# Kernel tuning notes

Measured on AMD Instinct MI355X. Metric: run time of the kernel, lower is better.

## Reference

```python
import jax, jax.numpy as jnp
import numpy as np

E, K, CAP = 8, 2, 48
RD, NC = 64, 10
LOAD_PEN, MIN_USE, TEMP = 2.0, 0.05, 1.0


def _conv(x, w):
    return jax.lax.conv_general_dilated(x, w, (1, 1), 'SAME',
                                        dimension_numbers=('NCHW', 'OIHW', 'NCHW'))


def _bn(x, g, b):
    # eval-mode BatchNorm2d with running_mean=0, running_var=1, eps=1e-5
    s = g / np.float32(np.sqrt(1.0 + 1e-5))
    return x * s[:, None, None] + b[:, None, None]


def _maxpool2(x):
    return jax.lax.reduce_window(x, -jnp.inf, jax.lax.max,
                                 (1, 1, 2, 2), (1, 1, 2, 2), 'VALID')


def setup_inputs() -> dict:
    key = jax.random.key(0)
    ks = iter(jax.random.split(key, 40))
    n = lambda shape, s=0.1: jax.random.normal(next(ks), shape, jnp.float32) * s
    B = 256
    return dict(
        x=jax.random.normal(next(ks), (B, 3, 32, 32), jnp.float32),
        # routing trunk
        tw1=n((32, 3, 3, 3)), tg1=jnp.ones(32), tb1=jnp.zeros(32),
        tw2=n((32, 32, 3, 3)), tg2=jnp.ones(32), tb2=jnp.zeros(32),
        tfw=n((RD, 128)), tfb=jnp.zeros(RD),
        # gate MLP
        gw1=n((RD // 2, RD)), gb1=jnp.zeros(RD // 2),
        gw2=n((E, RD // 2)), gb2=jnp.zeros(E),
        # per-expert feature extractors (stacked over E)
        ew1=n((E, 32, 3, 3, 3)), eg1=jnp.ones((E, 32)), eb1=jnp.zeros((E, 32)),
        ew2=n((E, 64, 32, 3, 3)), eg2=jnp.ones((E, 64)), eb2=jnp.zeros((E, 64)),
        ew3=n((E, 128, 64, 3, 3)), eg3=jnp.ones((E, 128)), eb3=jnp.zeros((E, 128)),
        efw=n((E, 128, 128)), efb=jnp.zeros((E, 128)),
        # per-expert classifiers (stacked over E)
        cw1=n((E, 64, 128)), cb1=jnp.zeros((E, 64)),
        cw2=n((E, NC, 64)), cb2=jnp.zeros((E, NC)),
    )


def _forward(x, tw1, tg1, tb1, tw2, tg2, tb2, tfw, tfb, gw1, gb1, gw2, gb2,
             ew1, eg1, eb1, ew2, eg2, eb2, ew3, eg3, eb3, efw, efb,
             cw1, cb1, cw2, cb2):
    B = x.shape[0]
    # ---- routing trunk ----
    h = jax.nn.relu(_bn(_conv(x, tw1), tg1, tb1))
    h = jax.nn.relu(_bn(_conv(h, tw2), tg2, tb2))
    h = _maxpool2(h)                                   # [B,32,16,16]
    h = h.reshape(B, 32, 2, 8, 2, 8).mean((3, 5))      # AdaptiveAvgPool2d(2)
    rf = jax.nn.relu(h.reshape(B, 128) @ tfw.T + tfb)  # [B,RD]
    # ---- gate ----
    scores = (jax.nn.relu(rf @ gw1.T + gb1) @ gw2.T + gb2) / TEMP  # [B,E]
    usage = jnp.ones(E, jnp.float32) / E               # expert_usage_ema buffer
    boost = jnp.where(usage < MIN_USE, (MIN_USE - usage) * 10.0, 0.0)
    balanced = scores + boost[None] - LOAD_PEN * usage[None]
    # ---- capacity-constrained top-k routing (eval: sample_order = arange) ----
    _, tk = jax.lax.top_k(balanced, K)                 # [B,K] int32

    def step(loads, tki):
        lt = loads[tki]                                # [K] loads of this sample's top-k
        avail = lt < CAP
        idx = jnp.where(jnp.any(avail), jnp.argmax(avail), jnp.argmin(lt))
        chosen = tki[idx]
        return loads.at[chosen].add(1.0), chosen

    _, chosen = jax.lax.scan(step, jnp.zeros(E, jnp.float32), tk)
    D = jax.nn.one_hot(chosen, E, dtype=bool)          # [B,E] dispatch mask

    # ---- experts: run each expert on the full batch, zero out unassigned ----
    def expert(w1, g1, b1, w2, g2, b2, w3, g3, b3, fw, fb, c1w, c1b, c2w, c2b):
        h = _maxpool2(jax.nn.relu(_bn(_conv(x, w1), g1, b1)))   # [B,32,16,16]
        h = _maxpool2(jax.nn.relu(_bn(_conv(h, w2), g2, b2)))   # [B,64,8,8]
        h = jax.nn.relu(_bn(_conv(h, w3), g3, b3)).mean((2, 3)) # GAP -> [B,128]
        f = jax.nn.relu(h @ fw.T + fb)
        return jax.nn.relu(f @ c1w.T + c1b) @ c2w.T + c2b        # [B,NC]

    outs = jax.vmap(expert)(ew1, eg1, eb1, ew2, eg2, eb2, ew3, eg3, eb3,
                            efw, efb, cw1, cb1, cw2, cb2)        # [E,B,NC]
    expert_outputs = jnp.where(D.T[:, :, None], outs, 0.0).transpose(1, 0, 2)  # [B,E,NC]

    # ---- combine via softmax over dispatched scores ----
    masked = jnp.where(D, balanced, -jnp.inf)
    rw = jax.nn.softmax(masked, axis=1) * D
    rw = rw / (rw.sum(1, keepdims=True) + 1e-12)
    final = jnp.einsum('be,bec->bc', rw, expert_outputs)         # [B,NC]
    return final, balanced, D


def reference(x, tw1, tg1, tb1, tw2, tg2, tb2, tfw, tfb, gw1, gb1, gw2, gb2,
              ew1, eg1, eb1, ew2, eg2, eb2, ew3, eg3, eb3, efw, efb,
              cw1, cb1, cw2, cb2):
    return _forward(x, tw1, tg1, tb1, tw2, tg2, tb2, tfw, tfb,
                    gw1, gb1, gw2, gb2, ew1, eg1, eb1, ew2, eg2, eb2,
                    ew3, eg3, eb3, efw, efb, cw1, cb1, cw2, cb2)
```

## Files before the change

kernel.cpp:

```cpp
#include <hip/hip_runtime.h>
#include <hip/hip_bf16.h>
#include <math.h>


#define BN_RS (1.0f / sqrtf(1.00001f))

typedef __attribute__((ext_vector_type(8))) short short8;
typedef __attribute__((ext_vector_type(4))) float floatx4;

static __device__ __forceinline__ ushort f2bf(float f) {
  unsigned u = __float_as_uint(f);
  unsigned r = (u + 0x7fffu + ((u >> 16) & 1u)) >> 16;
  return (ushort)r;
}
static __device__ __forceinline__ float bf2f(ushort h) {
  return __uint_as_float((unsigned)h << 16);
}

#define WS_TFP    0
#define WS_TK     262144
#define WS_W2H    264192
#define WS_W2L    282624
#define WS_EW2B   301056
#define WS_EW3B   595968

__global__ __launch_bounds__(256) void prep_kernel(
    const float* __restrict__ tw2, const float* __restrict__ ew2,
    const float* __restrict__ ew3, ushort* __restrict__ w2h,
    ushort* __restrict__ w2l, ushort* __restrict__ ew2b,
    ushort* __restrict__ ew3b)
{
  const int j = blockIdx.x * 256 + threadIdx.x;
  if (j < 9216) {
    int tap = j >> 10, oc = (j >> 5) & 31, ic = j & 31;
    float v = tw2[oc*288 + ic*9 + tap];
    ushort h = f2bf(v);
    w2h[j] = h;
    w2l[j] = f2bf(v - bf2f(h));
  } else if (j < 27648) {
    const int jj = (j - 9216) * 8;
    int e = jj / 18432, r2 = jj % 18432;
    int tap = r2 / 2048, r3 = r2 % 2048;
    int oc = r3 / 32, ic0 = r3 % 32;
    const float* src = &ew2[e*18432 + oc*288 + ic0*9 + tap];
    short8 o;
    #pragma unroll
    for (int k = 0; k < 8; ++k) o[k] = (short)f2bf(src[k*9]);
    *(short8*)&ew2b[jj] = o;
  } else if (j < 101376) {
    const int jj = (j - 27648) * 8;
    int e = jj / 73728, r2 = jj % 73728;
    int tap = r2 / 8192, r3 = r2 % 8192;
    int oc = r3 / 64, ic0 = r3 % 64;
    const float* src = &ew3[e*73728 + oc*576 + ic0*9 + tap];
    short8 o;
    #pragma unroll
    for (int k = 0; k < 8; ++k) o[k] = (short)f2bf(src[k*9]);
    *(short8*)&ew3b[jj] = o;
  }
}

__global__ __launch_bounds__(256) void trunk_kernel(
    const float* __restrict__ x, const float* __restrict__ tw1,
    const float* __restrict__ tg1, const float* __restrict__ tb1,
    const ushort* __restrict__ w2h, const ushort* __restrict__ w2l,
    const float* __restrict__ tg2, const float* __restrict__ tb2,
    float* __restrict__ tfp)
{
  __shared__ __align__(16) ushort smu[17696];
  float* smf = (float*)&smu[14400];
  const int t = threadIdx.x, blk = blockIdx.x;
  const int b = blk >> 3, rs = (blk >> 1) & 3, ch = blk & 1;
  const int r0 = rs * 8, c0 = ch * 16;

  {
    uint4 z = {0, 0, 0, 0};
    for (int j = t; j < 1800; j += 256) ((uint4*)smu)[j] = z;
  }
  for (int j = t; j < 720; j += 256) {
    int ic = j / 240, rem = j % 240, rr = rem / 20, c = rem % 20;
    int gy = r0 - 2 + rr, gx = c0 - 2 + c;
    float v = 0.f;
    if (gy >= 0 && gy < 32 && gx >= 0 && gx < 32)
      v = x[b*3072 + ic*1024 + gy*32 + gx];
    smf[j] = v;
  }
  for (int j = t; j < 864; j += 256) {
    int oc = j / 27, r = j % 27, ic = r / 9, k = r % 9;
    smf[720 + ic*288 + k*32 + oc] = tw1[j];
  }
  if (t < 32) { smf[1584 + t] = tg1[t]*BN_RS; smf[1584 + 32 + t] = tb1[t]; }
  __syncthreads();

  for (int it = 0; it < 2; ++it) {
    const int item = it*256 + t;
    if (item < 320) {
      const int oc = item & 31, rr = item >> 5;
      const int grow = r0 - 1 + rr;
      if (grow >= 0 && grow < 32) {
        float acc[18];
        #pragma unroll
        for (int c = 0; c < 18; ++c) acc[c] = 0.f;
        #pragma unroll 1
        for (int ic = 0; ic < 3; ++ic) {
          #pragma unroll 1
          for (int ky = 0; ky < 3; ++ky) {
            float wk[3];
            #pragma unroll
            for (int kx = 0; kx < 3; ++kx)
              wk[kx] = smf[720 + ic*288 + (ky*3 + kx)*32 + oc];
            const float* srow = &smf[ic*240 + (rr + ky)*20];
            float v[20];
            #pragma unroll
            for (int j4 = 0; j4 < 5; ++j4) {
              float4 q = *(const float4*)&srow[4*j4];
              v[4*j4] = q.x; v[4*j4+1] = q.y; v[4*j4+2] = q.z; v[4*j4+3] = q.w;
            }
            #pragma unroll
            for (int kx = 0; kx < 3; ++kx)
              #pragma unroll
              for (int c = 0; c < 18; ++c)
                acc[c] = fmaf(wk[kx], v[c+kx], acc[c]);
          }
        }
        const float s = smf[1584 + oc], bo = smf[1584 + 32 + oc];
        #pragma unroll
        for (int c = 0; c < 18; ++c) {
          const int gcol = c0 - 1 + c;
          float va = 0.f;
          if (gcol >= 0 && gcol < 32)
            va = fmaxf(fmaf(acc[c], s, bo), 0.f);
          ushort h = f2bf(va);
          ushort lo = f2bf(va - bf2f(h));
          const int ui = (rr*18 + c)*40 + oc;
          smu[ui] = h;
          smu[7200 + ui] = lo;
        }
      }
    }
  }
  __syncthreads();

  const int w4 = t >> 6, l = t & 63, col = l & 15, quad = l >> 4;
  const int nt = w4 & 1, yh = w4 >> 1;
  floatx4 acc2[4];
  #pragma unroll
  for (int y = 0; y < 4; ++y)
    #pragma unroll
    for (int i = 0; i < 4; ++i) acc2[y][i] = 0.f;

  #pragma unroll
  for (int dx = 0; dx < 3; ++dx) {
    #pragma unroll
    for (int dy = 0; dy < 3; ++dy) {
      const int wi = (dy*3 + dx)*1024 + (nt*16 + col)*32 + quad*8;
      short8 bh = *(const short8*)&w2h[wi];
      short8 bl = *(const short8*)&w2l[wi];
      #pragma unroll
      for (int y = 0; y < 4; ++y) {
        const int idx = ((yh*4 + y + dy)*18 + col + dx)*40 + quad*8;
        short8 ah = *(const short8*)&smu[idx];
        short8 al = *(const short8*)&smu[7200 + idx];
        acc2[y] = __builtin_amdgcn_mfma_f32_16x16x32_bf16(ah, bh, acc2[y], 0, 0, 0);
        acc2[y] = __builtin_amdgcn_mfma_f32_16x16x32_bf16(ah, bl, acc2[y], 0, 0, 0);
        acc2[y] = __builtin_amdgcn_mfma_f32_16x16x32_bf16(al, bh, acc2[y], 0, 0, 0);
      }
    }
  }

  {
    const int oc = nt*16 + col;
    const float s2 = tg2[oc]*BN_RS, bo2 = tb2[oc];
    float psum = 0.f;
    #pragma unroll
    for (int yp = 0; yp < 2; ++yp)
      #pragma unroll
      for (int i2 = 0; i2 < 2; ++i2) {
        float v00 = fmaxf(fmaf(acc2[2*yp][2*i2],     s2, bo2), 0.f);
        float v01 = fmaxf(fmaf(acc2[2*yp][2*i2+1],   s2, bo2), 0.f);
        float v10 = fmaxf(fmaf(acc2[2*yp+1][2*i2],   s2, bo2), 0.f);
        float v11 = fmaxf(fmaf(acc2[2*yp+1][2*i2+1], s2, bo2), 0.f);
        psum += fmaxf(fmaxf(v00, v01), fmaxf(v10, v11));
      }
    psum += __shfl_xor(psum, 16);
    psum += __shfl_xor(psum, 32);
    if (yh == 1 && quad == 0) smf[nt*32 + col] = psum;
    __syncthreads();
    if (yh == 0 && quad == 0) {
      float tot = psum + smf[nt*32 + col];
      tfp[b*256 + (rs*2 + ch)*32 + oc] = tot;
    }
  }
}

__global__ __launch_bounds__(64) void gate_kernel(
    const float* __restrict__ tfp, const float* __restrict__ tfw, const float* __restrict__ tfb,
    const float* __restrict__ gw1, const float* __restrict__ gb1,
    const float* __restrict__ gw2, const float* __restrict__ gb2,
    float* __restrict__ outBal, int* __restrict__ tk)
{
  __shared__ float feat[128], rf[64], g1[32], bal[8];
  const int b = blockIdx.x, t = threadIdx.x;
  #pragma unroll
  for (int h = 0; h < 2; ++h) {
    const int f = t + 64*h;
    const int oc = f >> 2, qy = (f >> 1) & 1, qx = f & 1;
    feat[f] = (tfp[b*256 + (4*qy + qx)*32 + oc] +
               tfp[b*256 + (4*qy + 2 + qx)*32 + oc]) * (1.f/64.f);
  }
  __syncthreads();
  {
    float a = tfb[t];
    const float4* wp = (const float4*)&tfw[t*128];
    #pragma unroll 8
    for (int i4 = 0; i4 < 32; ++i4) {
      float4 wv = wp[i4];
      a = fmaf(wv.x, feat[4*i4], a);   a = fmaf(wv.y, feat[4*i4+1], a);
      a = fmaf(wv.z, feat[4*i4+2], a); a = fmaf(wv.w, feat[4*i4+3], a);
    }
    rf[t] = fmaxf(a, 0.f);
  }
  __syncthreads();
  if (t < 32) {
    float a = gb1[t];
    const float4* wp = (const float4*)&gw1[t*64];
    #pragma unroll
    for (int i4 = 0; i4 < 16; ++i4) {
      float4 wv = wp[i4];
      a = fmaf(wv.x, rf[4*i4], a);   a = fmaf(wv.y, rf[4*i4+1], a);
      a = fmaf(wv.z, rf[4*i4+2], a); a = fmaf(wv.w, rf[4*i4+3], a);
    }
    g1[t] = fmaxf(a, 0.f);
  }
  __syncthreads();
  if (t < 8) {
    float a = gb2[t];
    const float4* wp = (const float4*)&gw2[t*32];
    #pragma unroll
    for (int i4 = 0; i4 < 8; ++i4) {
      float4 wv = wp[i4];
      a = fmaf(wv.x, g1[4*i4], a);   a = fmaf(wv.y, g1[4*i4+1], a);
      a = fmaf(wv.z, g1[4*i4+2], a); a = fmaf(wv.w, g1[4*i4+3], a);
    }
    const float v = a - 0.25f;
    bal[t] = v;
    outBal[b*8 + t] = v;
  }
  __syncthreads();
  if (t == 0) {
    int t0 = 0; float b0 = bal[0];
    #pragma unroll
    for (int e2 = 1; e2 < 8; ++e2) if (bal[e2] > b0) { b0 = bal[e2]; t0 = e2; }
    int t1 = -1; float b1 = -3.4e38f;
    #pragma unroll
    for (int e2 = 0; e2 < 8; ++e2) if (e2 != t0 && bal[e2] > b1) { b1 = bal[e2]; t1 = e2; }
    tk[b*2] = t0; tk[b*2 + 1] = t1;
  }
}

#define XA_IMG  0
#define XA_FEAT 3600
#define XA_SFF  3728
#define XA_SGG  3856
#define XA_XF   9040
#define XA_W1F  12508
#define XA_BN1F 13372
#define XA_SC   9040
__global__ __launch_bounds__(512, 2) void expALL_kernel(
    const float* __restrict__ x, const int* __restrict__ tk,
    const float* __restrict__ ew1, const float* __restrict__ eg1,
    const float* __restrict__ eb1, const ushort* __restrict__ ew2b,
    const float* __restrict__ eg2, const float* __restrict__ eb2,
    const ushort* __restrict__ ew3b, const float* __restrict__ eg3,
    const float* __restrict__ eb3, const float* __restrict__ efw,
    const float* __restrict__ efb, const float* __restrict__ cw1,
    const float* __restrict__ cb1, const float* __restrict__ cw2,
    const float* __restrict__ cb2, float* __restrict__ outF,
    float* __restrict__ outD)
{
  __shared__ __align__(16) ushort smu[27296];
  __shared__ int stk[512];
  __shared__ int sch;
  float* smf = (float*)smu;
  const int t = threadIdx.x, b = blockIdx.x;
  const int w8 = t >> 6, l = t & 63;
  const int col = l & 15, quad = l >> 4;

  stk[t] = tk[t];
  __syncthreads();
  if (t == 0) {
    unsigned long long Lp = 0ull;
    int chv = 0;
    for (int i = 0; i <= b; ++i) {
      const int a = stk[2*i], c = stk[2*i+1];
      const int la = (int)((Lp >> (a*8)) & 0xFFull);
      const int lc = (int)((Lp >> (c*8)) & 0xFFull);
      chv = (la < 48) ? a : ((lc < 48) ? c : ((la <= lc) ? a : c));
      Lp += 1ull << (chv*8);
    }
    sch = chv;
  } else {
    uint4 z; z.x = 0; z.y = 0; z.z = 0; z.w = 0;
    for (int j = t-1; j < 1620; j += 511) ((uint4*)smu)[j] = z;
    for (int j = t-1; j < 3468; j += 511) {
      int ic = j / 1156, rem = j % 1156, p = rem / 34, cpd = rem % 34;
      int gy = p - 1, gx = cpd - 1;
      float v = 0.f;
      if (gy >= 0 && gy < 32 && gx >= 0 && gx < 32) v = x[b*3072 + ic*1024 + gy*32 + gx];
      smf[XA_XF + j] = v;
    }
  }
  __syncthreads();
  const int e = sch;
  if (t < 8) outD[b*8 + t] = (t == e) ? 1.f : 0.f;

  const int ntile = w8 & 3, mhalf = w8 >> 2;
  short8 w2f[9];
  {
    const int oc2 = ntile*16 + col;
    #pragma unroll
    for (int tap = 0; tap < 9; ++tap)
      w2f[tap] = *(const short8*)&ew2b[(e*9 + tap)*2048 + oc2*32 + quad*8];
  }

  for (int j = t; j < 864; j += 512) {
    int oc = j / 27, r = j % 27, ic = r / 9, k = r % 9;
    smf[XA_W1F + ic*288 + k*32 + oc] = ew1[e*864 + j];
  }
  if (t < 32) { smf[XA_BN1F + t] = eg1[e*32 + t]*BN_RS; smf[XA_BN1F + 32 + t] = eb1[e*32 + t]; }
  __syncthreads();

  {
    const int g = t >> 5, c = t & 31;
    for (int rs = 0; rs < 4; ++rs) {
      const int r0 = rs * 8;
      float acc[2][8];
      #pragma unroll
      for (int o = 0; o < 2; ++o)
        #pragma unroll
        for (int r = 0; r < 8; ++r) acc[o][r] = 0.f;
      for (int ic = 0; ic < 3; ++ic) {
        float w[2][9];
        #pragma unroll
        for (int k = 0; k < 9; ++k) {
          float2 wv = *(const float2*)&smf[XA_W1F + ic*288 + k*32 + 2*g];
          w[0][k] = wv.x; w[1][k] = wv.y;
        }
        const float* src = &smf[XA_XF + ic*1156 + r0*34 + c];
        #pragma unroll
        for (int rr = 0; rr < 10; ++rr) {
          const float i0 = src[rr*34], i1 = src[rr*34 + 1], i2 = src[rr*34 + 2];
          #pragma unroll
          for (int dr = 0; dr < 3; ++dr) {
            const int r = rr - dr;
            if (r < 0 || r > 7) continue;
            #pragma unroll
            for (int o = 0; o < 2; ++o) {
              acc[o][r] = fmaf(w[o][dr*3+0], i0, acc[o][r]);
              acc[o][r] = fmaf(w[o][dr*3+1], i1, acc[o][r]);
              acc[o][r] = fmaf(w[o][dr*3+2], i2, acc[o][r]);
            }
          }
        }
      }
      #pragma unroll
      for (int o = 0; o < 2; ++o) {
        const int oc = 2*g + o;
        const float s = smf[XA_BN1F + oc], bo = smf[XA_BN1F + 32 + oc];
        float m[4];
        #pragma unroll
        for (int pr = 0; pr < 4; ++pr) {
          float v0 = fmaxf(fmaf(acc[o][2*pr],   s, bo), 0.f);
          float v1 = fmaxf(fmaf(acc[o][2*pr+1], s, bo), 0.f);
          m[pr] = fmaxf(v0, v1);
        }
        #pragma unroll
        for (int pr = 0; pr < 4; ++pr) {
          float nb = __shfl_xor(m[pr], 1);
          m[pr] = fmaxf(m[pr], nb);
        }
        if (!(c & 1)) {
          const int pc = c >> 1;
          #pragma unroll
          for (int pr = 0; pr < 4; ++pr)
            smu[XA_IMG + ((rs*4 + pr + 1)*18 + (pc + 1))*40 + oc] = f2bf(m[pr]);
        }
      }
    }
  }
  __syncthreads();

  const int oc3 = w8*16 + col;
  short8 w3f[9][2];
  #pragma unroll
  for (int tap = 0; tap < 9; ++tap)
    #pragma unroll
    for (int ks = 0; ks < 2; ++ks)
      w3f[tap][ks] = *(const short8*)&ew3b[(e*9 + tap)*8192 + oc3*64 + ks*32 + quad*8];

  {
    floatx4 acc[8];
    #pragma unroll
    for (int mt = 0; mt < 8; ++mt)
      #pragma unroll
      for (int i = 0; i < 4; ++i) acc[mt][i] = 0.f;

    #pragma unroll
    for (int tap = 0; tap < 9; ++tap) {
      const int dy = tap / 3, dx = tap % 3;
      #pragma unroll
      for (int mtl = 0; mtl < 8; ++mtl) {
        const int mt = mhalf*8 + mtl;
        short8 afr = *(const short8*)
            &smu[XA_IMG + ((mt + dy)*18 + col + dx)*40 + quad*8];
        acc[mtl] = __builtin_amdgcn_mfma_f32_16x16x32_bf16(afr, w2f[tap], acc[mtl], 0, 0, 0);
      }
    }
    __syncthreads();

    {
      uint4 z; z.x = 0; z.y = 0; z.z = 0; z.w = 0;
      for (int j = t; j < 288; j += 512) {
        int slot = j >> 3, ofs = (j & 7) * 8, row, cl;
        if (slot < 10)      { row = 0; cl = slot; }
        else if (slot < 20) { row = 9; cl = slot - 10; }
        else if (slot < 28) { row = 1 + (slot - 20); cl = 0; }
        else                { row = 1 + (slot - 28); cl = 9; }
        *(uint4*)&smu[(row*10 + cl)*72 + ofs] = z;
      }
    }
    const int oc2 = ntile*16 + col;
    const float s2 = eg2[e*64 + oc2]*BN_RS, bo2 = eb2[e*64 + oc2];
    #pragma unroll
    for (int mtpl = 0; mtpl < 4; ++mtpl) {
      const int mtp = mhalf*4 + mtpl;
      float a00 = fmaxf(fmaf(acc[2*mtpl][0],   s2, bo2), 0.f);
      float a01 = fmaxf(fmaf(acc[2*mtpl][1],   s2, bo2), 0.f);
      float a02 = fmaxf(fmaf(acc[2*mtpl][2],   s2, bo2), 0.f);
      float a03 = fmaxf(fmaf(acc[2*mtpl][3],   s2, bo2), 0.f);
      float a10 = fmaxf(fmaf(acc[2*mtpl+1][0], s2, bo2), 0.f);
      float a11 = fmaxf(fmaf(acc[2*mtpl+1][1], s2, bo2), 0.f);
      float a12 = fmaxf(fmaf(acc[2*mtpl+1][2], s2, bo2), 0.f);
      float a13 = fmaxf(fmaf(acc[2*mtpl+1][3], s2, bo2), 0.f);
      float p0 = fmaxf(fmaxf(a00, a01), fmaxf(a10, a11));
      float p1 = fmaxf(fmaxf(a02, a03), fmaxf(a12, a13));
      smu[((mtp + 1)*10 + (quad*2 + 1))*72 + oc2] = f2bf(p0);
      smu[((mtp + 1)*10 + (quad*2 + 2))*72 + oc2] = f2bf(p1);
    }
  }
  __syncthreads();

  const int fcout = t & 127, fcpart = t >> 7;
  float4 efr[8];
  {
    const float4* wp = (const float4*)&efw[e*16384 + fcout*128 + fcpart*32];
    #pragma unroll
    for (int i4 = 0; i4 < 8; ++i4) efr[i4] = wp[i4];
  }

  {
    floatx4 acc[4];
    #pragma unroll
    for (int mt = 0; mt < 4; ++mt)
      #pragma unroll
      for (int i = 0; i < 4; ++i) acc[mt][i] = 0.f;

    #pragma unroll
    for (int tap = 0; tap < 9; ++tap) {
      const int dy = tap / 3, dx = tap % 3;
      #pragma unroll
      for (int ks = 0; ks < 2; ++ks) {
        #pragma unroll
        for (int mt = 0; mt < 4; ++mt) {
          const int m = mt*16 + col;
          const int y = m >> 3, xx = m & 7;
          short8 afr = *(const short8*)
              &smu[((y + dy)*10 + (xx + dx))*72 + ks*32 + quad*8];
          acc[mt] = __builtin_amdgcn_mfma_f32_16x16x32_bf16(afr, w3f[tap][ks], acc[mt], 0, 0, 0);
        }
      }
    }

    {
      const float s = eg3[e*128 + oc3]*BN_RS, bo = eb3[e*128 + oc3];
      float gsum = 0.f;
      #pragma unroll
      for (int mt = 0; mt < 4; ++mt)
        #pragma unroll
        for (int i = 0; i < 4; ++i)
          gsum += fmaxf(fmaf(acc[mt][i], s, bo), 0.f);
      gsum += __shfl_xor(gsum, 16);
      gsum += __shfl_xor(gsum, 32);
      if (quad == 0) smf[XA_FEAT + oc3] = gsum * (1.f/64.f);
    }
  }
  __syncthreads();

  {
    float a = (fcpart == 0) ? efb[e*128 + fcout] : 0.f;
    #pragma unroll
    for (int i4 = 0; i4 < 8; ++i4) {
      float4 wv = efr[i4];
      const int base = XA_FEAT + fcpart*32 + 4*i4;
      a = fmaf(wv.x, smf[base], a);     a = fmaf(wv.y, smf[base + 1], a);
      a = fmaf(wv.z, smf[base + 2], a); a = fmaf(wv.w, smf[base + 3], a);
    }
    smf[XA_SC + fcpart*128 + fcout] = a;
  }
  __syncthreads();
  if (t < 128)
    smf[XA_SFF + t] = fmaxf(smf[XA_SC + t] + smf[XA_SC + 128 + t] +
                            smf[XA_SC + 256 + t] + smf[XA_SC + 384 + t], 0.f);
  __syncthreads();
  if (t < 256) {
    const int out = t & 63, part = t >> 6;
    float a = (part == 0) ? cb1[e*64 + out] : 0.f;
    const float4* wp = (const float4*)&cw1[e*8192 + out*128 + part*32];
    #pragma unroll
    for (int i4 = 0; i4 < 8; ++i4) {
      float4 wv = wp[i4];
      const int base = XA_SFF + part*32 + 4*i4;
      a = fmaf(wv.x, smf[base], a);     a = fmaf(wv.y, smf[base + 1], a);
      a = fmaf(wv.z, smf[base + 2], a); a = fmaf(wv.w, smf[base + 3], a);
    }
    smf[XA_SC + part*64 + out] = a;
  }
  __syncthreads();
  if (t < 64)
    smf[XA_SGG + t] = fmaxf(smf[XA_SC + t] + smf[XA_SC + 64 + t] +
                            smf[XA_SC + 128 + t] + smf[XA_SC + 192 + t], 0.f);
  __syncthreads();
  if (t < 10) {
    float a = cb2[e*10 + t];
    const float4* wp = (const float4*)&cw2[e*640 + t*64];
    #pragma unroll
    for (int i4 = 0; i4 < 16; ++i4) {
      float4 wv = wp[i4];
      a = fmaf(wv.x, smf[XA_SGG + 4*i4],     a);
      a = fmaf(wv.y, smf[XA_SGG + 4*i4 + 1], a);
      a = fmaf(wv.z, smf[XA_SGG + 4*i4 + 2], a);
      a = fmaf(wv.w, smf[XA_SGG + 4*i4 + 3], a);
    }
    outF[b*10 + t] = a;
  }
}

extern "C" void kernel_launch(void* const* d_in, const int* in_sizes, int n_in,
                              void* d_out, int out_size, void* d_ws, size_t ws_size,
                              hipStream_t stream)
{
  const float* x   = (const float*)d_in[0];
  const float* tw1 = (const float*)d_in[1];
  const float* tg1 = (const float*)d_in[2];
  const float* tb1 = (const float*)d_in[3];
  const float* tw2 = (const float*)d_in[4];
  const float* tg2 = (const float*)d_in[5];
  const float* tb2 = (const float*)d_in[6];
  const float* tfw = (const float*)d_in[7];
  const float* tfb = (const float*)d_in[8];
  const float* gw1 = (const float*)d_in[9];
  const float* gb1 = (const float*)d_in[10];
  const float* gw2 = (const float*)d_in[11];
  const float* gb2 = (const float*)d_in[12];
  const float* ew1 = (const float*)d_in[13];
  const float* eg1 = (const float*)d_in[14];
  const float* eb1 = (const float*)d_in[15];
  const float* ew2 = (const float*)d_in[16];
  const float* eg2 = (const float*)d_in[17];
  const float* eb2 = (const float*)d_in[18];
  const float* ew3 = (const float*)d_in[19];
  const float* eg3 = (const float*)d_in[20];
  const float* eb3 = (const float*)d_in[21];
  const float* efw = (const float*)d_in[22];
  const float* efb = (const float*)d_in[23];
  const float* cw1 = (const float*)d_in[24];
  const float* cb1 = (const float*)d_in[25];
  const float* cw2 = (const float*)d_in[26];
  const float* cb2 = (const float*)d_in[27];

  float*  out  = (float*)d_out;
  char*   ws   = (char*)d_ws;
  float*  tfp  = (float*)(ws + WS_TFP);
  int*    tk   = (int*)(ws + WS_TK);
  ushort* w2h  = (ushort*)(ws + WS_W2H);
  ushort* w2l  = (ushort*)(ws + WS_W2L);
  ushort* ew2b = (ushort*)(ws + WS_EW2B);
  ushort* ew3b = (ushort*)(ws + WS_EW3B);

  prep_kernel<<<396, 256, 0, stream>>>(tw2, ew2, ew3, w2h, w2l, ew2b, ew3b);
  trunk_kernel<<<2048, 256, 0, stream>>>(x, tw1, tg1, tb1, w2h, w2l, tg2, tb2, tfp);
  gate_kernel<<<256, 64, 0, stream>>>(tfp, tfw, tfb, gw1, gb1, gw2, gb2,
                                      out + 2560, tk);
  expALL_kernel<<<256, 512, 0, stream>>>(x, tk, ew1, eg1, eb1, ew2b, eg2, eb2,
                                         ew3b, eg3, eb3, efw, efb, cw1, cb1,
                                         cw2, cb2, out, out + 4608);
}
```

Before: 182.8 us.

## Move expert weight bf16 conversion into trunk kernel and batch gate blocks

```diff
diff --git a/kernel.cpp b/kernel.cpp
--- a/kernel.cpp
+++ b/kernel.cpp
@@ -25,39 +25,15 @@
 #define WS_EW3B   595968
 
 __global__ __launch_bounds__(256) void prep_kernel(
-    const float* __restrict__ tw2, const float* __restrict__ ew2,
-    const float* __restrict__ ew3, ushort* __restrict__ w2h,
-    ushort* __restrict__ w2l, ushort* __restrict__ ew2b,
-    ushort* __restrict__ ew3b)
+    const float* __restrict__ tw2, ushort* __restrict__ w2h,
+    ushort* __restrict__ w2l)
 {
   const int j = blockIdx.x * 256 + threadIdx.x;
-  if (j < 9216) {
-    int tap = j >> 10, oc = (j >> 5) & 31, ic = j & 31;
-    float v = tw2[oc*288 + ic*9 + tap];
-    ushort h = f2bf(v);
-    w2h[j] = h;
-    w2l[j] = f2bf(v - bf2f(h));
-  } else if (j < 27648) {
-    const int jj = (j - 9216) * 8;
-    int e = jj / 18432, r2 = jj % 18432;
-    int tap = r2 / 2048, r3 = r2 % 2048;
-    int oc = r3 / 32, ic0 = r3 % 32;
-    const float* src = &ew2[e*18432 + oc*288 + ic0*9 + tap];
-    short8 o;
-    #pragma unroll
-    for (int k = 0; k < 8; ++k) o[k] = (short)f2bf(src[k*9]);
-    *(short8*)&ew2b[jj] = o;
-  } else if (j < 101376) {
-    const int jj = (j - 27648) * 8;
-    int e = jj / 73728, r2 = jj % 73728;
-    int tap = r2 / 8192, r3 = r2 % 8192;
-    int oc = r3 / 64, ic0 = r3 % 64;
-    const float* src = &ew3[e*73728 + oc*576 + ic0*9 + tap];
-    short8 o;
-    #pragma unroll
-    for (int k = 0; k < 8; ++k) o[k] = (short)f2bf(src[k*9]);
-    *(short8*)&ew3b[jj] = o;
-  }
+  int tap = j >> 10, oc = (j >> 5) & 31, ic = j & 31;
+  float v = tw2[oc*288 + ic*9 + tap];
+  ushort h = f2bf(v);
+  w2h[j] = h;
+  w2l[j] = f2bf(v - bf2f(h));
 }
 
 __global__ __launch_bounds__(256) void trunk_kernel(
@@ -65,6 +41,8 @@
     const float* __restrict__ tg1, const float* __restrict__ tb1,
     const ushort* __restrict__ w2h, const ushort* __restrict__ w2l,
     const float* __restrict__ tg2, const float* __restrict__ tb2,
+    const float* __restrict__ ew2, const float* __restrict__ ew3,
+    ushort* __restrict__ ew2b, ushort* __restrict__ ew3b,
     float* __restrict__ tfp)
 {
   __shared__ __align__(16) ushort smu[17696];
@@ -72,6 +50,31 @@
   const int t = threadIdx.x, blk = blockIdx.x;
   const int b = blk >> 3, rs = (blk >> 1) & 3, ch = blk & 1;
   const int r0 = rs * 8, c0 = ch * 16;
+
+  if (t < 45) {
+    const int item = blk * 45 + t;
+    if (item < 18432) {
+      const int jj = item * 8;
+      int e = jj / 18432, r2 = jj % 18432;
+      int tap = r2 / 2048, r3 = r2 % 2048;
+      int oc = r3 / 32, ic0 = r3 % 32;
+      const float* src = &ew2[e*18432 + oc*288 + ic0*9 + tap];
+      short8 o;
+      #pragma unroll
+      for (int k = 0; k < 8; ++k) o[k] = (short)f2bf(src[k*9]);
+      *(short8*)&ew2b[jj] = o;
+    } else {
+      const int jj = (item - 18432) * 8;
+      int e = jj / 73728, r2 = jj % 73728;
+      int tap = r2 / 8192, r3 = r2 % 8192;
+      int oc = r3 / 64, ic0 = r3 % 64;
+      const float* src = &ew3[e*73728 + oc*576 + ic0*9 + tap];
+      short8 o;
+      #pragma unroll
+      for (int k = 0; k < 8; ++k) o[k] = (short)f2bf(src[k*9]);
+      *(short8*)&ew3b[jj] = o;
+    }
+  }
 
   {
     uint4 z = {0, 0, 0, 0};
@@ -193,20 +196,21 @@
   }
 }
 
-__global__ __launch_bounds__(64) void gate_kernel(
+__global__ __launch_bounds__(512) void gate_kernel(
     const float* __restrict__ tfp, const float* __restrict__ tfw, const float* __restrict__ tfb,
     const float* __restrict__ gw1, const float* __restrict__ gb1,
     const float* __restrict__ gw2, const float* __restrict__ gb2,
     float* __restrict__ outBal, int* __restrict__ tk)
 {
-  __shared__ float feat[128], rf[64], g1[32], bal[8];
-  const int b = blockIdx.x, t = threadIdx.x;
+  __shared__ float feat[8][128], rf[8][64], g1[8][32], bal[8][8];
+  const int grp = threadIdx.x >> 6, t = threadIdx.x & 63;
+  const int b = blockIdx.x * 8 + grp;
   #pragma unroll
   for (int h = 0; h < 2; ++h) {
     const int f = t + 64*h;
     const int oc = f >> 2, qy = (f >> 1) & 1, qx = f & 1;
-    feat[f] = (tfp[b*256 + (4*qy + qx)*32 + oc] +
-               tfp[b*256 + (4*qy + 2 + qx)*32 + oc]) * (1.f/64.f);
+    feat[grp][f] = (tfp[b*256 + (4*qy + qx)*32 + oc] +
+                    tfp[b*256 + (4*qy + 2 + qx)*32 + oc]) * (1.f/64.f);
   }
   __syncthreads();
   {
@@ -215,10 +219,10 @@
     #pragma unroll 8
     for (int i4 = 0; i4 < 32; ++i4) {
       float4 wv = wp[i4];
-      a = fmaf(wv.x, feat[4*i4], a);   a = fmaf(wv.y, feat[4*i4+1], a);
-      a = fmaf(wv.z, feat[4*i4+2], a); a = fmaf(wv.w, feat[4*i4+3], a);
-    }
-    rf[t] = fmaxf(a, 0.f);
+      a = fmaf(wv.x, feat[grp][4*i4], a);   a = fmaf(wv.y, feat[grp][4*i4+1], a);
+      a = fmaf(wv.z, feat[grp][4*i4+2], a); a = fmaf(wv.w, feat[grp][4*i4+3], a);
+    }
+    rf[grp][t] = fmaxf(a, 0.f);
   }
   __syncthreads();
   if (t < 32) {
@@ -227,10 +231,10 @@
     #pragma unroll
     for (int i4 = 0; i4 < 16; ++i4) {
       float4 wv = wp[i4];
-      a = fmaf(wv.x, rf[4*i4], a);   a = fmaf(wv.y, rf[4*i4+1], a);
-      a = fmaf(wv.z, rf[4*i4+2], a); a = fmaf(wv.w, rf[4*i4+3], a);
-    }
-    g1[t] = fmaxf(a, 0.f);
+      a = fmaf(wv.x, rf[grp][4*i4], a);   a = fmaf(wv.y, rf[grp][4*i4+1], a);
+      a = fmaf(wv.z, rf[grp][4*i4+2], a); a = fmaf(wv.w, rf[grp][4*i4+3], a);
+    }
+    g1[grp][t] = fmaxf(a, 0.f);
   }
   __syncthreads();
   if (t < 8) {
@@ -239,21 +243,21 @@
     #pragma unroll
     for (int i4 = 0; i4 < 8; ++i4) {
       float4 wv = wp[i4];
-      a = fmaf(wv.x, g1[4*i4], a);   a = fmaf(wv.y, g1[4*i4+1], a);
-      a = fmaf(wv.z, g1[4*i4+2], a); a = fmaf(wv.w, g1[4*i4+3], a);
+      a = fmaf(wv.x, g1[grp][4*i4], a);   a = fmaf(wv.y, g1[grp][4*i4+1], a);
+      a = fmaf(wv.z, g1[grp][4*i4+2], a); a = fmaf(wv.w, g1[grp][4*i4+3], a);
     }
     const float v = a - 0.25f;
-    bal[t] = v;
+    bal[grp][t] = v;
     outBal[b*8 + t] = v;
   }
   __syncthreads();
   if (t == 0) {
-    int t0 = 0; float b0 = bal[0];
-    #pragma unroll
-    for (int e2 = 1; e2 < 8; ++e2) if (bal[e2] > b0) { b0 = bal[e2]; t0 = e2; }
+    int t0 = 0; float b0 = bal[grp][0];
+    #pragma unroll
+    for (int e2 = 1; e2 < 8; ++e2) if (bal[grp][e2] > b0) { b0 = bal[grp][e2]; t0 = e2; }
     int t1 = -1; float b1 = -3.4e38f;
     #pragma unroll
-    for (int e2 = 0; e2 < 8; ++e2) if (e2 != t0 && bal[e2] > b1) { b1 = bal[e2]; t1 = e2; }
+    for (int e2 = 0; e2 < 8; ++e2) if (e2 != t0 && bal[grp][e2] > b1) { b1 = bal[grp][e2]; t1 = e2; }
     tk[b*2] = t0; tk[b*2 + 1] = t1;
   }
 }
@@ -587,9 +591,10 @@
   ushort* ew2b = (ushort*)(ws + WS_EW2B);
   ushort* ew3b = (ushort*)(ws + WS_EW3B);
 
-  prep_kernel<<<396, 256, 0, stream>>>(tw2, ew2, ew3, w2h, w2l, ew2b, ew3b);
-  trunk_kernel<<<2048, 256, 0, stream>>>(x, tw1, tg1, tb1, w2h, w2l, tg2, tb2, tfp);
-  gate_kernel<<<256, 64, 0, stream>>>(tfp, tfw, tfb, gw1, gb1, gw2, gb2,
+  prep_kernel<<<36, 256, 0, stream>>>(tw2, w2h, w2l);
+  trunk_kernel<<<2048, 256, 0, stream>>>(x, tw1, tg1, tb1, w2h, w2l, tg2, tb2,
+                                         ew2, ew3, ew2b, ew3b, tfp);
+  gate_kernel<<<32, 512, 0, stream>>>(tfp, tfw, tfb, gw1, gb1, gw2, gb2,
                                       out + 2560, tk);
   expALL_kernel<<<256, 512, 0, stream>>>(x, tk, ew1, eg1, eb1, ew2b, eg2, eb2,
                                          ew3b, eg3, eb3, efw, efb, cw1, cb1,
```

Measured after the change: 193.0 us. 5.6% more time.
